# Kernel optimization log

Hardware: AMD Instinct MI355X
Metric: run time of the kernel (lower is better)

The kernel has to match this reference:

```python
import jax, jax.numpy as jnp
import numpy as np

TS = 1.5          # hard-coded sampling period in forward()
W_CENTER = 337.927  # hard-coded center frequency in forward()


def shg_mat(yta):
    """Vectorized createSHGmat: yta is a complex64 vector of length N.
    Row m: Ts * fftshift(fft(fftshift(yta * roll(yta, delay[m]) * shiftFactor))).
    torch.roll(x, s)[j] == x[(j - s) % N], matching the gather below."""
    N = yta.shape[0]
    delays_f = jnp.arange(-(N // 2), N // 2, dtype=jnp.float32)
    delays_i = jnp.arange(-(N // 2), N // 2, dtype=jnp.int32)
    shift_factor = jnp.exp(-1j * 2.0 * W_CENTER * TS * delays_f).astype(jnp.complex64)  # [N]
    idx = (jnp.arange(N, dtype=jnp.int32)[None, :] - delays_i[:, None]) % N  # [N, N]
    y_shift = yta[idx]                                    # [N(delay), N(elem)]
    prod = yta[None, :] * y_shift * shift_factor[None, :]  # elementwise, [N, N]
    prod = jnp.fft.fftshift(prod, axes=-1)
    mat = TS * jnp.fft.fftshift(jnp.fft.fft(prod, axis=-1), axes=-1)
    return mat  # complex64 [N, N]


def frog_error(Tref, Tmeas):
    """calcFrogError: scalar FROG error between reference and measured traces."""
    mu = jnp.sum(Tmeas @ Tref) / jnp.sum(Tref @ Tref)
    r = jnp.sum((Tmeas - mu * Tref) ** 2)
    norm = jnp.float32(Tmeas.size) * jnp.max(Tmeas) ** 2
    return jnp.sqrt(r / norm)


def setup_inputs() -> dict:
    key = jax.random.key(0)
    k1, k2, k3 = jax.random.split(key, 3)
    B, N = 8, 1024
    prediction = jax.random.normal(k1, (B, 2 * N), dtype=jnp.float32)
    label = jax.random.normal(k2, (B, 2 * N), dtype=jnp.float32)
    spectrogram = jax.random.uniform(k3, (N, N), dtype=jnp.float32)
    return {"prediction": prediction, "label": label, "spectrogram": spectrogram}


def reference(prediction, label, spectrogram):
    B, two_n = prediction.shape
    n = two_n // 2
    pred_analytical = (prediction[:, :n] + 1j * prediction[:, n:]).astype(jnp.complex64)  # [B, N]
    mats = jax.vmap(shg_mat)(pred_analytical)          # [B, N, N] complex64
    Tref = jnp.abs(mats)                               # predicted SHG trace magnitude
    errs = jax.vmap(lambda t: frog_error(t, spectrogram))(Tref)  # [B]
    # loss = (sum over batch of frog_error) / batch_size; masked MSE terms in the
    # original are computed but never added to the returned loss, so they are omitted.
    return jnp.mean(errs)
```

## Files before the change

### kernel.cpp

```cpp
#include <hip/hip_runtime.h>
#include <math.h>

#define N 1024
#define B_ 8
#define T_ 256
#define R_ 4
#define NREP 4
#define GX 129

#define OFF_SF      0
#define OFF_TW      2048
#define OFF_ROWSUM  10240
#define ZERO_START  18432
#define OFF_COLSUMM 18432
#define OFF_SUMM2   19456
#define OFF_MAXM    19457
#define OFF_SUMMT   19464
#define OFF_SUMTT   19472
#define OFF_COLT    20480
#define WS_END      (OFF_COLT + B_ * NREP * N)

#define S1(a) ((a) ^ (((a) >> 2) & 0x10))
#define S2(a) ((a) ^ (((a) >> 3) & 0x0C))
#define S3(a) ((a) ^ (((a) >> 5) & 0x07))
#define S4(a) ((a) ^ (((a) >> 5) & 0x07))

__device__ __forceinline__ float wave_sum(float v) {
    #pragma unroll
    for (int o = 32; o > 0; o >>= 1) v += __shfl_down(v, o, 64);
    return v;
}
__device__ __forceinline__ float wave_max(float v) {
    #pragma unroll
    for (int o = 32; o > 0; o >>= 1) v = fmaxf(v, __shfl_down(v, o, 64));
    return v;
}

__device__ __forceinline__ void load_tw(float tw[6], const float* __restrict__ p) {
    float4 v = *(const float4*)p;
    float2 w = *(const float2*)(p + 4);
    tw[0] = v.x; tw[1] = v.y; tw[2] = v.z; tw[3] = v.w; tw[4] = w.x; tw[5] = w.y;
}

__device__ __forceinline__ void bfly4(float xr[4], float xi[4], const float tw[6]) {
    float t0r = xr[0] + xr[2], t0i = xi[0] + xi[2];
    float t1r = xr[0] - xr[2], t1i = xi[0] - xi[2];
    float t2r = xr[1] + xr[3], t2i = xi[1] + xi[3];
    float t3r = xr[1] - xr[3], t3i = xi[1] - xi[3];
    float y1r = t1r + t3i, y1i = t1i - t3r;
    float y2r = t0r - t2r, y2i = t0i - t2i;
    float y3r = t1r - t3i, y3i = t1i + t3r;
    xr[0] = t0r + t2r;            xi[0] = t0i + t2i;
    xr[1] = y1r * tw[0] - y1i * tw[1]; xi[1] = y1r * tw[1] + y1i * tw[0];
    xr[2] = y2r * tw[2] - y2i * tw[3]; xi[2] = y2r * tw[3] + y2i * tw[2];
    xr[3] = y3r * tw[4] - y3i * tw[5]; xi[3] = y3r * tw[5] + y3i * tw[4];
}

__global__ __launch_bounds__(T_) void k_prep(float* ws, float* out) {
    const int e = blockIdx.x * T_ + threadIdx.x;
    {
        double ang = -2.0 * 337.927 * 1.5 * (double)(e - 512);
        double s, c;
        sincos(ang, &s, &c);
        ws[OFF_SF + 2 * e] = (float)c;
        ws[OFF_SF + 2 * e + 1] = (float)s;
    }
    {
        int s = e >> 8, tt = e & 255;
        int h = 256 >> (2 * s);
        int pos = tt & (h - 1);
        int step = 1 << (2 * s);
        double a1 = -2.0 * M_PI * (double)(pos * step) / 1024.0;
        double s1, c1, s2, c2, s3, c3;
        sincos(a1, &s1, &c1);
        sincos(2.0 * a1, &s2, &c2);
        sincos(3.0 * a1, &s3, &c3);
        float* p = ws + OFF_TW + e * 8;
        p[0] = (float)c1; p[1] = (float)s1;
        p[2] = (float)c2; p[3] = (float)s2;
        p[4] = (float)c3; p[5] = (float)s3;
        p[6] = 0.f; p[7] = 0.f;
    }
    for (int j = ZERO_START + e; j < WS_END; j += 4 * T_) ws[j] = 0.f;
    if (e == 0) out[0] = 0.f;
}

__global__ __launch_bounds__(T_, 6) void k_row(const float* __restrict__ pred,
                                               const float* __restrict__ M,
                                               float* __restrict__ ws) {
    __shared__ float Yr[N], Yi[N];
    __shared__ float Ar[N], Ai[N], Br[N], Bi[N];
    __shared__ float colA[N];
    __shared__ float red[R_ + 2][4];
    const int t = threadIdx.x;
    const int blk = blockIdx.x;
    const int b = blockIdx.y;
    const int wid = t >> 6, lane = t & 63;

    if (b == B_) {
        if (blk >= 64) return;
        const int r0 = blk * 16;
        float cs[4] = {0.f, 0.f, 0.f, 0.f};
        float sq = 0.f, mx = 0.f;
        for (int r = 0; r < 16; ++r) {
            const float* row = M + (size_t)(r0 + r) * N;
            #pragma unroll
            for (int q = 0; q < 4; ++q) {
                float v = row[t + T_ * q];
                cs[q] += v;
                sq += v * v;
                mx = fmaxf(mx, v);
            }
        }
        #pragma unroll
        for (int q = 0; q < 4; ++q) atomicAdd(&ws[OFF_COLSUMM + t + T_ * q], cs[q]);
        sq = wave_sum(sq);
        mx = wave_max(mx);
        if (lane == 0) { red[0][wid] = sq; red[1][wid] = mx; }
        __syncthreads();
        if (t == 0) {
            atomicAdd(&ws[OFF_SUMM2], red[0][0] + red[0][1] + red[0][2] + red[0][3]);
            float X = fmaxf(fmaxf(red[1][0], red[1][1]), fmaxf(red[1][2], red[1][3]));
            atomicMax((unsigned int*)ws + OFF_MAXM, __float_as_uint(X));
        }
        return;
    }

    const int nr = (blk == GX - 1) ? 1 : R_;
    const int m0 = blk * R_;

    {
        const float* pr = pred + (size_t)b * 2 * N;
        #pragma unroll
        for (int q = 0; q < 4; ++q) {
            int j = t + T_ * q;
            Yr[j] = pr[j];
            Yi[j] = pr[N + j];
            colA[j] = 0.f;
        }
    }

    float tw0[6], tw1[6], tw2[6], tw3[6];
    load_tw(tw0, ws + OFF_TW + (size_t)t * 8);
    load_tw(tw1, ws + OFF_TW + (size_t)(256 + t) * 8);
    load_tw(tw2, ws + OFF_TW + (size_t)(512 + t) * 8);
    load_tw(tw3, ws + OFF_TW + (size_t)(768 + t) * 8);
    __syncthreads();

    float mtacc = 0.f, ttacc = 0.f;
    float xr[4], xi[4];

    for (int r = 0; r < nr; ++r) {
        const int m = m0 + r;
        const int mm = (N - m) & (N - 1);
        const float w = (mm == m) ? 1.f : 2.f;

        {
            const float2* sf2 = (const float2*)(ws + OFF_SF);
            #pragma unroll
            for (int q = 0; q < 4; ++q) {
                int j = t + T_ * q;
                int s = (j - m + 512) & (N - 1);
                float ar = Yr[j], ai = Yi[j];
                float br = Yr[s], bi = Yi[s];
                float2 sv = sf2[j];
                float p_r = ar * br - ai * bi;
                float p_i = ar * bi + ai * br;
                xr[q] = p_r * sv.x - p_i * sv.y;
                xi[q] = p_r * sv.y + p_i * sv.x;
            }
            bfly4(xr, xi, tw0);
            #pragma unroll
            for (int q = 0; q < 4; ++q) { int a = t + 256 * q; Ar[a] = xr[q]; Ai[a] = xi[q]; }
        }
        __syncthreads();

        {
            int base = ((t >> 6) << 8) | (t & 63);
            #pragma unroll
            for (int q = 0; q < 4; ++q) { int a = base + (q << 6); xr[q] = Ar[a]; xi[q] = Ai[a]; }
            bfly4(xr, xi, tw1);
            #pragma unroll
            for (int q = 0; q < 4; ++q) { int a = S1(base + (q << 6)); Br[a] = xr[q]; Bi[a] = xi[q]; }
        }
        __syncthreads();

        {
            int base = ((t >> 4) << 6) | (t & 15);
            #pragma unroll
            for (int q = 0; q < 4; ++q) { int a = S1(base + (q << 4)); xr[q] = Br[a]; xi[q] = Bi[a]; }
            bfly4(xr, xi, tw2);
            #pragma unroll
            for (int q = 0; q < 4; ++q) { int a = S2(base + (q << 4)); Ar[a] = xr[q]; Ai[a] = xi[q]; }
        }
        __syncthreads();

        {
            int base = ((t >> 2) << 4) | (t & 3);
            #pragma unroll
            for (int q = 0; q < 4; ++q) { int a = S2(base + (q << 2)); xr[q] = Ar[a]; xi[q] = Ai[a]; }
            bfly4(xr, xi, tw3);
            #pragma unroll
            for (int q = 0; q < 4; ++q) { int a = S3(base + (q << 2)); Br[a] = xr[q]; Bi[a] = xi[q]; }
        }
        __syncthreads();

        {
            int base = t << 2;
            #pragma unroll
            for (int q = 0; q < 4; ++q) { int a = S3(base + q); xr[q] = Br[a]; xi[q] = Bi[a]; }
            float t0r = xr[0] + xr[2], t0i = xi[0] + xi[2];
            float t1r = xr[0] - xr[2], t1i = xi[0] - xi[2];
            float t2r = xr[1] + xr[3], t2i = xi[1] + xi[3];
            float t3r = xr[1] - xr[3], t3i = xi[1] - xi[3];
            float yr[4], yi[4];
            yr[0] = t0r + t2r; yi[0] = t0i + t2i;
            yr[1] = t1r + t3i; yi[1] = t1i - t3r;
            yr[2] = t0r - t2r; yi[2] = t0i - t2i;
            yr[3] = t1r - t3i; yi[3] = t1i + t3r;
            int r4t = ((t & 3) << 6) | (((t >> 2) & 3) << 4) | (((t >> 4) & 3) << 2) | ((t >> 6) & 3);
            #pragma unroll
            for (int q = 0; q < 4; ++q) {
                int c = ((q << 8) | r4t) ^ 512;
                Ar[S4(c)] = 1.5f * sqrtf(yr[q] * yr[q] + yi[q] * yi[q]);
            }
        }
        __syncthreads();

        {
            const float* Mrow = M + (size_t)m * N;
            const float* Mrow2 = M + (size_t)mm * N;
            float rs = 0.f;
            #pragma unroll
            for (int q = 0; q < 4; ++q) {
                int cc = t + 256 * q;
                float v = Ar[S4(cc)];
                rs += v;
                ttacc += w * v * v;
                float msum = Mrow[cc];
                if (mm != m) msum += Mrow2[cc];
                mtacc += msum * v;
                colA[cc] += w * v;
            }
            rs = wave_sum(rs);
            if (lane == 0) red[r][wid] = rs;
        }
        __syncthreads();
    }

    {
        float* colT = ws + OFF_COLT + (size_t)(b * NREP + (blk & (NREP - 1))) * N;
        #pragma unroll
        for (int q = 0; q < 4; ++q) {
            int cc = t + 256 * q;
            atomicAdd(&colT[cc], colA[cc]);
        }
        float mt = wave_sum(mtacc);
        float tt2 = wave_sum(ttacc);
        if (lane == 0) { red[R_][wid] = mt; red[R_ + 1][wid] = tt2; }
        __syncthreads();
        if (t == 0) {
            for (int r = 0; r < nr; ++r) {
                int m = m0 + r, mm = (N - m) & (N - 1);
                float R = red[r][0] + red[r][1] + red[r][2] + red[r][3];
                ws[OFF_ROWSUM + b * N + m] = R;
                if (mm != m) ws[OFF_ROWSUM + b * N + mm] = R;
            }
            atomicAdd(&ws[OFF_SUMMT + b], red[R_][0] + red[R_][1] + red[R_][2] + red[R_][3]);
            atomicAdd(&ws[OFF_SUMTT + b], red[R_ + 1][0] + red[R_ + 1][1] + red[R_ + 1][2] + red[R_ + 1][3]);
        }
    }
}

__global__ __launch_bounds__(T_) void k_final(float* ws, float* out) {
    __shared__ double redn[4], redd[4];
    const int b = blockIdx.x;
    const int t = threadIdx.x;
    const int wid = t >> 6, lane = t & 63;
    const float* rowsum = ws + OFF_ROWSUM + (size_t)b * N;
    double num = 0.0, den = 0.0;
    #pragma unroll
    for (int q = 0; q < 4; ++q) {
        int j = t + 256 * q;
        double r = (double)rowsum[j];
        float ct = 0.f;
        #pragma unroll
        for (int rep = 0; rep < NREP; ++rep)
            ct += ws[OFF_COLT + (size_t)(b * NREP + rep) * N + j];
        num += (double)ws[OFF_COLSUMM + j] * r;
        den += (double)ct * r;
    }
    #pragma unroll
    for (int o = 32; o > 0; o >>= 1) {
        num += __shfl_down(num, o, 64);
        den += __shfl_down(den, o, 64);
    }
    if (lane == 0) { redn[wid] = num; redd[wid] = den; }
    __syncthreads();
    if (t == 0) {
        double NUM = redn[0] + redn[1] + redn[2] + redn[3];
        double DEN = redd[0] + redd[1] + redd[2] + redd[3];
        double mu = NUM / DEN;
        double r = (double)ws[OFF_SUMM2] - 2.0 * mu * (double)ws[OFF_SUMMT + b]
                 + mu * mu * (double)ws[OFF_SUMTT + b];
        float mx = ws[OFF_MAXM];
        double norm = 1048576.0 * (double)mx * (double)mx;
        atomicAdd(out, (float)(sqrt(r / norm) / 8.0));
    }
}

extern "C" void kernel_launch(void* const* d_in, const int* in_sizes, int n_in,
                              void* d_out, int out_size, void* d_ws, size_t ws_size,
                              hipStream_t stream) {
    const float* pred = (const float*)d_in[0];
    const float* M = (const float*)d_in[2];
    float* ws = (float*)d_ws;
    float* out = (float*)d_out;

    k_prep<<<4, T_, 0, stream>>>(ws, out);
    dim3 grid(GX, B_ + 1);
    k_row<<<grid, T_, 0, stream>>>(pred, M, ws);
    k_final<<<B_, T_, 0, stream>>>(ws, out);
}
```

Measured before the change: 100.7 us.

## Compute each 1024-point FFT per wavefront with register radix-16 and DPP final stage

The row FFT no longer uses a block-wide radix-4 scheme with five barrier-separated shared-memory passes. Each wavefront now computes whole rows itself: two register-resident radix-16 passes joined by one transpose through per-wave shared memory, then a final radix-4 stage done with DPP lane exchanges. The shift factor is pre-multiplied into a second copy of the input, and twiddles come from new precomputed tables. This removes block-level syncs and most LDS traffic per row. In exchange it needs more registers (launch bounds lowered to 3), uses a grid of 64 chunks with 8 rows each, and does more global atomics per thread for the column sums.

```diff
diff --git a/kernel.cpp b/kernel.cpp
--- a/kernel.cpp
+++ b/kernel.cpp
@@ -4,26 +4,21 @@
 #define N 1024
 #define B_ 8
 #define T_ 256
-#define R_ 4
 #define NREP 4
-#define GX 129
+#define CHUNKS 64
 
 #define OFF_SF      0
-#define OFF_TW      2048
-#define OFF_ROWSUM  10240
-#define ZERO_START  18432
-#define OFF_COLSUMM 18432
-#define OFF_SUMM2   19456
-#define OFF_MAXM    19457
-#define OFF_SUMMT   19464
-#define OFF_SUMTT   19472
-#define OFF_COLT    20480
+#define OFF_TA      2048
+#define OFF_TB      6144
+#define OFF_ROWSUM  6272
+#define ZERO_START  14464
+#define OFF_COLSUMM 14464
+#define OFF_SUMM2   15488
+#define OFF_MAXM    15489
+#define OFF_SUMMT   15496
+#define OFF_SUMTT   15504
+#define OFF_COLT    15520
 #define WS_END      (OFF_COLT + B_ * NREP * N)
-
-#define S1(a) ((a) ^ (((a) >> 2) & 0x10))
-#define S2(a) ((a) ^ (((a) >> 3) & 0x0C))
-#define S3(a) ((a) ^ (((a) >> 5) & 0x07))
-#define S4(a) ((a) ^ (((a) >> 5) & 0x07))
 
 __device__ __forceinline__ float wave_sum(float v) {
     #pragma unroll
@@ -36,87 +31,112 @@
     return v;
 }
 
-__device__ __forceinline__ void load_tw(float tw[6], const float* __restrict__ p) {
-    float4 v = *(const float4*)p;
-    float2 w = *(const float2*)(p + 4);
-    tw[0] = v.x; tw[1] = v.y; tw[2] = v.z; tw[3] = v.w; tw[4] = w.x; tw[5] = w.y;
-}
-
-__device__ __forceinline__ void bfly4(float xr[4], float xi[4], const float tw[6]) {
-    float t0r = xr[0] + xr[2], t0i = xi[0] + xi[2];
-    float t1r = xr[0] - xr[2], t1i = xi[0] - xi[2];
-    float t2r = xr[1] + xr[3], t2i = xi[1] + xi[3];
-    float t3r = xr[1] - xr[3], t3i = xi[1] - xi[3];
-    float y1r = t1r + t3i, y1i = t1i - t3r;
-    float y2r = t0r - t2r, y2i = t0i - t2i;
-    float y3r = t1r - t3i, y3i = t1i + t3r;
-    xr[0] = t0r + t2r;            xi[0] = t0i + t2i;
-    xr[1] = y1r * tw[0] - y1i * tw[1]; xi[1] = y1r * tw[1] + y1i * tw[0];
-    xr[2] = y2r * tw[2] - y2i * tw[3]; xi[2] = y2r * tw[3] + y2i * tw[2];
-    xr[3] = y3r * tw[4] - y3i * tw[5]; xi[3] = y3r * tw[5] + y3i * tw[4];
-}
+__device__ __forceinline__ void cmul(float& xr, float& xi, float wr, float wi) {
+    float r = xr * wr - xi * wi;
+    float i = xr * wi + xi * wr;
+    xr = r; xi = i;
+}
+
+__device__ __forceinline__ void dft4(float& r0, float& i0, float& r1, float& i1,
+                                     float& r2, float& i2, float& r3, float& i3) {
+    float e0r = r0 + r2, e0i = i0 + i2;
+    float e1r = r0 - r2, e1i = i0 - i2;
+    float e2r = r1 + r3, e2i = i1 + i3;
+    float e3r = r1 - r3, e3i = i1 - i3;
+    r0 = e0r + e2r; i0 = e0i + e2i;
+    r2 = e0r - e2r; i2 = e0i - e2i;
+    r1 = e1r + e3i; i1 = e1i - e3r;
+    r3 = e1r - e3i; i3 = e1i + e3r;
+}
+
+__device__ __forceinline__ void dft16(float xr[16], float xi[16]) {
+    #pragma unroll
+    for (int b = 0; b < 4; ++b)
+        dft4(xr[b], xi[b], xr[4 + b], xi[4 + b], xr[8 + b], xi[8 + b], xr[12 + b], xi[12 + b]);
+    const float C1 = 0.9238795325112867f, S1 = 0.3826834323650898f;
+    const float C2 = 0.7071067811865476f;
+    cmul(xr[5],  xi[5],   C1, -S1);
+    cmul(xr[6],  xi[6],   C2, -C2);
+    cmul(xr[7],  xi[7],   S1, -C1);
+    cmul(xr[9],  xi[9],   C2, -C2);
+    { float t = xr[10]; xr[10] = xi[10]; xi[10] = -t; }
+    cmul(xr[11], xi[11], -C2, -C2);
+    cmul(xr[13], xi[13],  S1, -C1);
+    cmul(xr[14], xi[14], -C2, -C2);
+    cmul(xr[15], xi[15], -C1,  S1);
+    #pragma unroll
+    for (int c = 0; c < 4; ++c)
+        dft4(xr[4 * c], xi[4 * c], xr[4 * c + 1], xi[4 * c + 1],
+             xr[4 * c + 2], xi[4 * c + 2], xr[4 * c + 3], xi[4 * c + 3]);
+}
+
+template<int CTRL>
+__device__ __forceinline__ float dppf(float x) {
+    return __int_as_float(__builtin_amdgcn_update_dpp(
+        0, __float_as_int(x), CTRL, 0xF, 0xF, true));
+}
+#define DPP_XOR1 0xB1
+#define DPP_XOR2 0x4E
 
 __global__ __launch_bounds__(T_) void k_prep(float* ws, float* out) {
     const int e = blockIdx.x * T_ + threadIdx.x;
-    {
+    if (e < 1024) {
         double ang = -2.0 * 337.927 * 1.5 * (double)(e - 512);
         double s, c;
         sincos(ang, &s, &c);
-        ws[OFF_SF + 2 * e] = (float)c;
+        ws[OFF_SF + 2 * e]     = (float)c;
         ws[OFF_SF + 2 * e + 1] = (float)s;
-    }
-    {
-        int s = e >> 8, tt = e & 255;
-        int h = 256 >> (2 * s);
-        int pos = tt & (h - 1);
-        int step = 1 << (2 * s);
-        double a1 = -2.0 * M_PI * (double)(pos * step) / 1024.0;
-        double s1, c1, s2, c2, s3, c3;
-        sincos(a1, &s1, &c1);
-        sincos(2.0 * a1, &s2, &c2);
-        sincos(3.0 * a1, &s3, &c3);
-        float* p = ws + OFF_TW + e * 8;
-        p[0] = (float)c1; p[1] = (float)s1;
-        p[2] = (float)c2; p[3] = (float)s2;
-        p[4] = (float)c3; p[5] = (float)s3;
-        p[6] = 0.f; p[7] = 0.f;
-    }
-    for (int j = ZERO_START + e; j < WS_END; j += 4 * T_) ws[j] = 0.f;
+    } else if (e < 2048) {
+        int e2 = e - 1024;
+        int k1 = e2 >> 6, uu = e2 & 63;
+        double ang = -2.0 * M_PI * (double)(uu * k1) / 1024.0;
+        double s, c;
+        sincos(ang, &s, &c);
+        ws[OFF_TA + 2 * e2]     = (float)c;
+        ws[OFF_TA + 2 * e2 + 1] = (float)s;
+    } else if (e < 2112) {
+        int e2 = e - 2048;
+        int k2 = e2 >> 2, n3 = e2 & 3;
+        double ang = -2.0 * M_PI * (double)(n3 * k2) / 64.0;
+        double s, c;
+        sincos(ang, &s, &c);
+        ws[OFF_TB + 2 * e2]     = (float)c;
+        ws[OFF_TB + 2 * e2 + 1] = (float)s;
+    }
+    for (int j = ZERO_START + e; j < WS_END; j += 12 * T_) ws[j] = 0.f;
     if (e == 0) out[0] = 0.f;
 }
 
-__global__ __launch_bounds__(T_, 6) void k_row(const float* __restrict__ pred,
+__global__ __launch_bounds__(T_, 3) void k_row(const float* __restrict__ pred,
                                                const float* __restrict__ M,
                                                float* __restrict__ ws) {
-    __shared__ float Yr[N], Yi[N];
-    __shared__ float Ar[N], Ai[N], Br[N], Bi[N];
-    __shared__ float colA[N];
-    __shared__ float red[R_ + 2][4];
+    __shared__ float2 Y2[N];
+    __shared__ float2 Ysf2[N];
+    __shared__ float2 TP[4][N];
+    __shared__ float2 TB2[64];
+    __shared__ float red[2][4];
     const int t = threadIdx.x;
-    const int blk = blockIdx.x;
+    const int cnk = blockIdx.x;
     const int b = blockIdx.y;
-    const int wid = t >> 6, lane = t & 63;
+    const int wid = t >> 6, u = t & 63;
 
     if (b == B_) {
-        if (blk >= 64) return;
-        const int r0 = blk * 16;
-        float cs[4] = {0.f, 0.f, 0.f, 0.f};
-        float sq = 0.f, mx = 0.f;
+        const int r0 = cnk * 16;
+        float cs0 = 0.f, cs1 = 0.f, cs2 = 0.f, cs3 = 0.f, sq = 0.f, mx = 0.f;
         for (int r = 0; r < 16; ++r) {
             const float* row = M + (size_t)(r0 + r) * N;
-            #pragma unroll
-            for (int q = 0; q < 4; ++q) {
-                float v = row[t + T_ * q];
-                cs[q] += v;
-                sq += v * v;
-                mx = fmaxf(mx, v);
-            }
-        }
-        #pragma unroll
-        for (int q = 0; q < 4; ++q) atomicAdd(&ws[OFF_COLSUMM + t + T_ * q], cs[q]);
+            float v0 = row[t], v1 = row[t + 256], v2 = row[t + 512], v3 = row[t + 768];
+            cs0 += v0; cs1 += v1; cs2 += v2; cs3 += v3;
+            sq += v0 * v0 + v1 * v1 + v2 * v2 + v3 * v3;
+            mx = fmaxf(mx, fmaxf(fmaxf(v0, v1), fmaxf(v2, v3)));
+        }
+        atomicAdd(&ws[OFF_COLSUMM + t],       cs0);
+        atomicAdd(&ws[OFF_COLSUMM + t + 256], cs1);
+        atomicAdd(&ws[OFF_COLSUMM + t + 512], cs2);
+        atomicAdd(&ws[OFF_COLSUMM + t + 768], cs3);
         sq = wave_sum(sq);
         mx = wave_max(mx);
-        if (lane == 0) { red[0][wid] = sq; red[1][wid] = mx; }
+        if (u == 0) { red[0][wid] = sq; red[1][wid] = mx; }
         __syncthreads();
         if (t == 0) {
             atomicAdd(&ws[OFF_SUMM2], red[0][0] + red[0][1] + red[0][2] + red[0][3]);
@@ -126,149 +146,135 @@
         return;
     }
 
-    const int nr = (blk == GX - 1) ? 1 : R_;
-    const int m0 = blk * R_;
-
     {
         const float* pr = pred + (size_t)b * 2 * N;
-        #pragma unroll
-        for (int q = 0; q < 4; ++q) {
-            int j = t + T_ * q;
-            Yr[j] = pr[j];
-            Yi[j] = pr[N + j];
-            colA[j] = 0.f;
-        }
-    }
-
-    float tw0[6], tw1[6], tw2[6], tw3[6];
-    load_tw(tw0, ws + OFF_TW + (size_t)t * 8);
-    load_tw(tw1, ws + OFF_TW + (size_t)(256 + t) * 8);
-    load_tw(tw2, ws + OFF_TW + (size_t)(512 + t) * 8);
-    load_tw(tw3, ws + OFF_TW + (size_t)(768 + t) * 8);
+        float4 re = *(const float4*)(pr + 4 * t);
+        float4 im = *(const float4*)(pr + N + 4 * t);
+        const float4* sfp = (const float4*)(ws + OFF_SF);
+        float4 sA = sfp[2 * t], sB = sfp[2 * t + 1];
+        int j0 = 4 * t;
+        Y2[j0 + 0] = make_float2(re.x, im.x);
+        Y2[j0 + 1] = make_float2(re.y, im.y);
+        Y2[j0 + 2] = make_float2(re.z, im.z);
+        Y2[j0 + 3] = make_float2(re.w, im.w);
+        Ysf2[j0 + 0] = make_float2(re.x * sA.x - im.x * sA.y, re.x * sA.y + im.x * sA.x);
+        Ysf2[j0 + 1] = make_float2(re.y * sA.z - im.y * sA.w, re.y * sA.w + im.y * sA.z);
+        Ysf2[j0 + 2] = make_float2(re.z * sB.x - im.z * sB.y, re.z * sB.y + im.z * sB.x);
+        Ysf2[j0 + 3] = make_float2(re.w * sB.z - im.w * sB.w, re.w * sB.w + im.w * sB.z);
+        if (t < 64) TB2[t] = ((const float2*)(ws + OFF_TB))[t];
+    }
+    float tar[16], tai[16];
+    {
+        const float2* taT = (const float2*)(ws + OFF_TA);
+        #pragma unroll
+        for (int r = 1; r < 16; ++r) {
+            int k1 = ((r & 3) << 2) | (r >> 2);
+            float2 wv = taT[(k1 << 6) + u];
+            tar[r] = wv.x; tai[r] = wv.y;
+        }
+    }
     __syncthreads();
 
-    float mtacc = 0.f, ttacc = 0.f;
-    float xr[4], xi[4];
-
-    for (int r = 0; r < nr; ++r) {
-        const int m = m0 + r;
+    const int k1u = u >> 2;
+    const int n3 = u & 3;
+    const int k3 = ((u & 1) << 1) | ((u >> 1) & 1);
+    const int clane = (k1u | (k3 << 8)) ^ 512;
+    const bool hi2 = (u & 2) != 0;
+    const bool odd = (u & 1) != 0;
+    float2* tp = TP[wid];
+
+    float colr[16];
+    #pragma unroll
+    for (int r = 0; r < 16; ++r) colr[r] = 0.f;
+    float mtl = 0.f, ttl = 0.f;
+
+    const int base = cnk * 8 + wid * 2;
+    const int nrow = (cnk == CHUNKS - 1 && wid == 0) ? 3 : 2;
+
+    for (int rr = 0; rr < nrow; ++rr) {
+        const int m = (rr < 2) ? (base + rr) : 512;
         const int mm = (N - m) & (N - 1);
         const float w = (mm == m) ? 1.f : 2.f;
 
-        {
-            const float2* sf2 = (const float2*)(ws + OFF_SF);
-            #pragma unroll
-            for (int q = 0; q < 4; ++q) {
-                int j = t + T_ * q;
-                int s = (j - m + 512) & (N - 1);
-                float ar = Yr[j], ai = Yi[j];
-                float br = Yr[s], bi = Yi[s];
-                float2 sv = sf2[j];
-                float p_r = ar * br - ai * bi;
-                float p_i = ar * bi + ai * br;
-                xr[q] = p_r * sv.x - p_i * sv.y;
-                xi[q] = p_r * sv.y + p_i * sv.x;
-            }
-            bfly4(xr, xi, tw0);
-            #pragma unroll
-            for (int q = 0; q < 4; ++q) { int a = t + 256 * q; Ar[a] = xr[q]; Ai[a] = xi[q]; }
-        }
-        __syncthreads();
-
-        {
-            int base = ((t >> 6) << 8) | (t & 63);
-            #pragma unroll
-            for (int q = 0; q < 4; ++q) { int a = base + (q << 6); xr[q] = Ar[a]; xi[q] = Ai[a]; }
-            bfly4(xr, xi, tw1);
-            #pragma unroll
-            for (int q = 0; q < 4; ++q) { int a = S1(base + (q << 6)); Br[a] = xr[q]; Bi[a] = xi[q]; }
-        }
-        __syncthreads();
-
-        {
-            int base = ((t >> 4) << 6) | (t & 15);
-            #pragma unroll
-            for (int q = 0; q < 4; ++q) { int a = S1(base + (q << 4)); xr[q] = Br[a]; xi[q] = Bi[a]; }
-            bfly4(xr, xi, tw2);
-            #pragma unroll
-            for (int q = 0; q < 4; ++q) { int a = S2(base + (q << 4)); Ar[a] = xr[q]; Ai[a] = xi[q]; }
-        }
-        __syncthreads();
-
-        {
-            int base = ((t >> 2) << 4) | (t & 3);
-            #pragma unroll
-            for (int q = 0; q < 4; ++q) { int a = S2(base + (q << 2)); xr[q] = Ar[a]; xi[q] = Ai[a]; }
-            bfly4(xr, xi, tw3);
-            #pragma unroll
-            for (int q = 0; q < 4; ++q) { int a = S3(base + (q << 2)); Br[a] = xr[q]; Bi[a] = xi[q]; }
-        }
-        __syncthreads();
-
-        {
-            int base = t << 2;
-            #pragma unroll
-            for (int q = 0; q < 4; ++q) { int a = S3(base + q); xr[q] = Br[a]; xi[q] = Bi[a]; }
-            float t0r = xr[0] + xr[2], t0i = xi[0] + xi[2];
-            float t1r = xr[0] - xr[2], t1i = xi[0] - xi[2];
-            float t2r = xr[1] + xr[3], t2i = xi[1] + xi[3];
-            float t3r = xr[1] - xr[3], t3i = xi[1] - xi[3];
-            float yr[4], yi[4];
-            yr[0] = t0r + t2r; yi[0] = t0i + t2i;
-            yr[1] = t1r + t3i; yi[1] = t1i - t3r;
-            yr[2] = t0r - t2r; yi[2] = t0i - t2i;
-            yr[3] = t1r - t3i; yi[3] = t1i + t3r;
-            int r4t = ((t & 3) << 6) | (((t >> 2) & 3) << 4) | (((t >> 4) & 3) << 2) | ((t >> 6) & 3);
-            #pragma unroll
-            for (int q = 0; q < 4; ++q) {
-                int c = ((q << 8) | r4t) ^ 512;
-                Ar[S4(c)] = 1.5f * sqrtf(yr[q] * yr[q] + yi[q] * yi[q]);
-            }
-        }
-        __syncthreads();
-
-        {
-            const float* Mrow = M + (size_t)m * N;
-            const float* Mrow2 = M + (size_t)mm * N;
-            float rs = 0.f;
-            #pragma unroll
-            for (int q = 0; q < 4; ++q) {
-                int cc = t + 256 * q;
-                float v = Ar[S4(cc)];
-                rs += v;
-                ttacc += w * v * v;
-                float msum = Mrow[cc];
-                if (mm != m) msum += Mrow2[cc];
-                mtacc += msum * v;
-                colA[cc] += w * v;
-            }
-            rs = wave_sum(rs);
-            if (lane == 0) red[r][wid] = rs;
-        }
-        __syncthreads();
-    }
-
-    {
-        float* colT = ws + OFF_COLT + (size_t)(b * NREP + (blk & (NREP - 1))) * N;
-        #pragma unroll
-        for (int q = 0; q < 4; ++q) {
-            int cc = t + 256 * q;
-            atomicAdd(&colT[cc], colA[cc]);
-        }
-        float mt = wave_sum(mtacc);
-        float tt2 = wave_sum(ttacc);
-        if (lane == 0) { red[R_][wid] = mt; red[R_ + 1][wid] = tt2; }
-        __syncthreads();
-        if (t == 0) {
-            for (int r = 0; r < nr; ++r) {
-                int m = m0 + r, mm = (N - m) & (N - 1);
-                float R = red[r][0] + red[r][1] + red[r][2] + red[r][3];
-                ws[OFF_ROWSUM + b * N + m] = R;
-                if (mm != m) ws[OFF_ROWSUM + b * N + mm] = R;
-            }
-            atomicAdd(&ws[OFF_SUMMT + b], red[R_][0] + red[R_][1] + red[R_][2] + red[R_][3]);
-            atomicAdd(&ws[OFF_SUMTT + b], red[R_ + 1][0] + red[R_ + 1][1] + red[R_ + 1][2] + red[R_ + 1][3]);
-        }
+        float xr[16], xi[16];
+        const int sbase = (u - m + 512) & (N - 1);
+        #pragma unroll
+        for (int n1 = 0; n1 < 16; ++n1) {
+            float2 a = Ysf2[(n1 << 6) + u];
+            int s = (sbase + (n1 << 6)) & (N - 1);
+            float2 yb = Y2[s];
+            xr[n1] = a.x * yb.x - a.y * yb.y;
+            xi[n1] = a.x * yb.y + a.y * yb.x;
+        }
+        dft16(xr, xi);
+        #pragma unroll
+        for (int r = 1; r < 16; ++r) cmul(xr[r], xi[r], tar[r], tai[r]);
+
+        asm volatile("s_waitcnt lgkmcnt(0)" ::: "memory");
+        #pragma unroll
+        for (int r = 0; r < 16; ++r) {
+            int k1 = ((r & 3) << 2) | (r >> 2);
+            int el = (k1 << 6) | (((k1u ^ k1) & 15) << 2) | n3;
+            tp[el] = make_float2(xr[r], xi[r]);
+        }
+        asm volatile("s_waitcnt lgkmcnt(0)" ::: "memory");
+        #pragma unroll
+        for (int n2 = 0; n2 < 16; ++n2) {
+            int el = (k1u << 6) | (((n2 ^ k1u) & 15) << 2) | n3;
+            float2 v = tp[el];
+            xr[n2] = v.x; xi[n2] = v.y;
+        }
+
+        dft16(xr, xi);
+        #pragma unroll
+        for (int r = 1; r < 16; ++r) {
+            int k2 = ((r & 3) << 2) | (r >> 2);
+            float2 wv = TB2[(k2 << 2) | n3];
+            cmul(xr[r], xi[r], wv.x, wv.y);
+        }
+
+        const float* Mrow  = M + (size_t)m * N + clane;
+        const float* Mrow2 = M + (size_t)mm * N + clane;
+        const bool domm = (mm != m);
+        const float w225 = w * 2.25f;
+        float rs = 0.f;
+        #pragma unroll
+        for (int r = 0; r < 16; ++r) {
+            int k2 = ((r & 3) << 2) | (r >> 2);
+            float ar = xr[r], ai = xi[r];
+            float br = dppf<DPP_XOR2>(ar), bi = dppf<DPP_XOR2>(ai);
+            float zr = hi2 ? (br - ar) : (ar + br);
+            float zi = hi2 ? (bi - ai) : (ai + bi);
+            float qr = dppf<DPP_XOR1>(zr), qi = dppf<DPP_XOR1>(zi);
+            float Xr = odd ? (qr - (hi2 ? zi : zr)) : (zr + (hi2 ? qi : qr));
+            float Xi = odd ? (qi + (hi2 ? zr : -zi)) : (zi + (hi2 ? -qr : qi));
+            float mag2 = Xr * Xr + Xi * Xi;
+            float v = 1.5f * sqrtf(mag2);
+            rs  += v;
+            ttl += w225 * mag2;
+            float ms = Mrow[k2 << 4];
+            if (domm) ms += Mrow2[k2 << 4];
+            mtl += ms * v;
+            colr[r] += w * v;
+        }
+        rs = wave_sum(rs);
+        if (u == 0) {
+            ws[OFF_ROWSUM + (size_t)b * N + m] = rs;
+            if (mm != m) ws[OFF_ROWSUM + (size_t)b * N + mm] = rs;
+        }
+    }
+
+    mtl = wave_sum(mtl);
+    ttl = wave_sum(ttl);
+    if (u == 0) {
+        atomicAdd(&ws[OFF_SUMMT + b], mtl);
+        atomicAdd(&ws[OFF_SUMTT + b], ttl);
+    }
+    float* colT = ws + OFF_COLT + (size_t)(b * NREP + (cnk & (NREP - 1))) * N;
+    #pragma unroll
+    for (int r = 0; r < 16; ++r) {
+        int k2 = ((r & 3) << 2) | (r >> 2);
+        atomicAdd(&colT[clane + (k2 << 4)], colr[r]);
     }
 }
 
@@ -317,8 +323,8 @@
     float* ws = (float*)d_ws;
     float* out = (float*)d_out;
 
-    k_prep<<<4, T_, 0, stream>>>(ws, out);
-    dim3 grid(GX, B_ + 1);
+    k_prep<<<12, T_, 0, stream>>>(ws, out);
+    dim3 grid(CHUNKS, B_ + 1);
     k_row<<<grid, T_, 0, stream>>>(pred, M, ws);
     k_final<<<B_, T_, 0, stream>>>(ws, out);
 }
```

Measured after the change: 121.3 us. 1.2x slower.
